# Kernel tuning notes

Hardware: AMD Instinct MI355X
Metric: run time of the kernel (lower is better)

The kernel has to match this reference:

```python
import jax, jax.numpy as jnp
import numpy as np

B, S, M, E, H, F, V, L = 2, 2048, 1024, 512, 8, 2048, 8192, 6


def setup_inputs() -> dict:
    key = jax.random.key(0)
    ks = iter(jax.random.split(key, 32))
    n = lambda shape, s=0.02: jax.random.normal(next(ks), shape, jnp.float32) * s
    return {
        "encoded": jax.random.normal(next(ks), (B, M, E), jnp.float32),
        "seq": jax.random.randint(next(ks), (B, S), 0, V, jnp.int32),
        "input_embed": n((V, E)),           # shared input/output embedding
        "pos_embed": n((S, E)),
        "output_bias": jnp.zeros((V,), jnp.float32),
        "self_in_w": n((L, 3 * E, E)), "self_in_b": jnp.zeros((L, 3 * E), jnp.float32),
        "self_out_w": n((L, E, E)), "self_out_b": jnp.zeros((L, E), jnp.float32),
        "cross_in_w": n((L, 3 * E, E)), "cross_in_b": jnp.zeros((L, 3 * E), jnp.float32),
        "cross_out_w": n((L, E, E)), "cross_out_b": jnp.zeros((L, E), jnp.float32),
        "self_norm_g": jnp.ones((L, E), jnp.float32), "self_norm_b": jnp.zeros((L, E), jnp.float32),
        "cross_norm_g": jnp.ones((L, E), jnp.float32), "cross_norm_b": jnp.zeros((L, E), jnp.float32),
        "mlp_norm_g": jnp.ones((L, E), jnp.float32), "mlp_norm_b": jnp.zeros((L, E), jnp.float32),
        "lin1_w": n((L, F, E)), "lin1_b": jnp.zeros((L, F), jnp.float32),
        "lin2_w": n((L, E, F)), "lin2_b": jnp.zeros((L, E), jnp.float32),
        "final_norm_g": jnp.ones((E,), jnp.float32), "final_norm_b": jnp.zeros((E,), jnp.float32),
    }


def _ln(x, g, b, eps=1e-5):
    m = jnp.mean(x, axis=-1, keepdims=True)
    v = jnp.mean((x - m) ** 2, axis=-1, keepdims=True)
    return (x - m) * jax.lax.rsqrt(v + eps) * g + b


def _mha(q, k, v, in_w, in_b, out_w, out_b, mask):
    # torch nn.MultiheadAttention (batch_first) with packed in_proj [3E, E]
    Ed = q.shape[-1]
    dh = Ed // H
    qp = q @ in_w[:Ed].T + in_b[:Ed]
    kp = k @ in_w[Ed:2 * Ed].T + in_b[Ed:2 * Ed]
    vp = v @ in_w[2 * Ed:].T + in_b[2 * Ed:]
    split = lambda t: t.reshape(t.shape[0], t.shape[1], H, dh).transpose(0, 2, 1, 3)
    qh, kh, vh = split(qp), split(kp), split(vp)  # [B, H, S, dh]
    scores = jnp.einsum('bhqd,bhkd->bhqk', qh, kh) / jnp.sqrt(jnp.float32(dh))
    if mask is not None:
        scores = jnp.where(mask, scores, jnp.float32(-1e9))
    attn = jax.nn.softmax(scores, axis=-1)
    o = jnp.einsum('bhqk,bhkd->bhqd', attn, vh)
    o = o.transpose(0, 2, 1, 3).reshape(q.shape[0], q.shape[1], Ed)
    return o @ out_w.T + out_b


def reference(encoded, seq, input_embed, pos_embed, output_bias,
              self_in_w, self_in_b, self_out_w, self_out_b,
              cross_in_w, cross_in_b, cross_out_w, cross_out_b,
              self_norm_g, self_norm_b, cross_norm_g, cross_norm_b,
              mlp_norm_g, mlp_norm_b, lin1_w, lin1_b, lin2_w, lin2_b,
              final_norm_g, final_norm_b):
    # TransformerDecoder.fit: teacher-forced forward (eval-mode dropout = identity)
    seq_len = seq.shape[1]
    x = input_embed[seq] + pos_embed[:seq_len]          # [B, S, E]
    causal = jnp.tril(jnp.ones((seq_len, seq_len), bool))
    for i in range(L):
        # post-norm decoder layer (norm_first=False)
        attn = _mha(x, x, x, self_in_w[i], self_in_b[i], self_out_w[i], self_out_b[i], causal)
        y = _ln(x + attn, self_norm_g[i], self_norm_b[i])
        cattn = _mha(y, encoded, encoded, cross_in_w[i], cross_in_b[i], cross_out_w[i], cross_out_b[i], None)
        y = _ln(y + cattn, cross_norm_g[i], cross_norm_b[i])
        h = jax.nn.gelu(y @ lin1_w[i].T + lin1_b[i], approximate=False)
        x = _ln(y + h @ lin2_w[i].T + lin2_b[i], mlp_norm_g[i], mlp_norm_b[i])
    x = _ln(x, final_norm_g, final_norm_b)               # decoder-final norm
    return x @ input_embed.T + output_bias               # shared output embedding
```

## Files before the change

kernel.cpp:

```cpp
#include <hip/hip_runtime.h>
#include <math.h>

typedef unsigned short u16;
typedef __attribute__((ext_vector_type(8))) unsigned short u16x8;
typedef __attribute__((ext_vector_type(8))) __bf16 bf16x8;
typedef __attribute__((ext_vector_type(4))) float f32x4;

constexpr int Bc = 2, Sc = 2048, Mc = 1024, Ec = 512, Hc = 8, DH = 64, Fc = 2048, Vc = 8192, Lc = 6;
constexpr int Nc = Bc * Sc;
constexpr int NMc = Bc * Mc;

__device__ __forceinline__ u16 f2b(float f) {
  __bf16 h = (__bf16)f;
  return __builtin_bit_cast(u16, h);
}

__device__ __forceinline__ f32x4 mfma16(bf16x8 a, bf16x8 b, f32x4 c) {
  return __builtin_amdgcn_mfma_f32_16x16x32_bf16(a, b, c, 0, 0, 0);
}

constexpr int C0 = 1179648;
constexpr int C1 = C0 + 393216;
constexpr int C2 = C1 + 1179648;
constexpr int C3 = C2 + 393216;
constexpr int C4 = C3 + 1572864;
constexpr int C5 = C4 + 1572864;
constexpr int C6 = C5 + 1048576;
constexpr int C7 = C6 + 262144;

__global__ __launch_bounds__(256) void k_cvt_all(
    const float* __restrict__ s0, const float* __restrict__ s1,
    const float* __restrict__ s2, const float* __restrict__ s3,
    const float* __restrict__ s4, const float* __restrict__ s5,
    const float* __restrict__ s6, const float* __restrict__ s7,
    u16* __restrict__ d0, u16* __restrict__ d1, u16* __restrict__ d2,
    u16* __restrict__ d3, u16* __restrict__ d4, u16* __restrict__ d5,
    u16* __restrict__ d6, u16* __restrict__ d7) {
  int i = blockIdx.x * 256 + threadIdx.x;
  const float* s; u16* d; int off;
  if (i < C3) {
    if (i < C1) { if (i < C0) { s = s0; d = d0; off = i; }
                  else        { s = s1; d = d1; off = i - C0; } }
    else        { if (i < C2) { s = s2; d = d2; off = i - C1; }
                  else        { s = s3; d = d3; off = i - C2; } }
  } else {
    if (i < C5) { if (i < C4) { s = s4; d = d4; off = i - C3; }
                  else        { s = s5; d = d5; off = i - C4; } }
    else        { if (i < C6) { s = s6; d = d6; off = i - C5; }
                  else        { s = s7; d = d7; off = i - C6; } }
  }
  float4 v = ((const float4*)s)[off];
  unsigned lo = (unsigned)f2b(v.x) | ((unsigned)f2b(v.y) << 16);
  unsigned hi = (unsigned)f2b(v.z) | ((unsigned)f2b(v.w) << 16);
  ((uint2*)d)[off] = make_uint2(lo, hi);
}

__global__ __launch_bounds__(256) void k_embed(const int* __restrict__ seq,
                                               const float* __restrict__ emb,
                                               const float* __restrict__ pos,
                                               float* __restrict__ x,
                                               u16* __restrict__ xb) {
  int idx = blockIdx.x * 256 + threadIdx.x;
  int row = idx >> 9, e = idx & 511;
  int s = row & (Sc - 1);
  float v = emb[(size_t)seq[row] * Ec + e] + pos[(size_t)s * Ec + e];
  x[idx] = v;
  xb[idx] = f2b(v);
}

template <int BM, int BN, int ACT>
__global__ __launch_bounds__(256) void k_gemm_bf(const u16* __restrict__ A,
                                                 const u16* __restrict__ W,
                                                 const float* __restrict__ bias,
                                                 float* __restrict__ C32,
                                                 u16* __restrict__ Cb,
                                                 int K, int Mo) {
  constexpr int WM = BM / 2, WN = BN / 2, FM = WM / 16, FN = WN / 16;
  __shared__ __attribute__((aligned(16))) u16 As[2][BM * 64];
  __shared__ __attribute__((aligned(16))) u16 Bs[2][BN * 64];
  const int tid = threadIdx.x;
  const int w = tid >> 6, l = tid & 63, l15 = l & 15, l4 = l >> 4;
  const int lr = l >> 3, lc = l & 7;
  const int wr = (w >> 1) * WM, wc = (w & 1) * WN;
  const size_t row0 = (size_t)blockIdx.y * BM, col0 = (size_t)blockIdx.x * BN;
  const u16* Ab = A + row0 * K;
  const u16* Wb = W + col0 * K;
  f32x4 acc[FM][FN] = {};

  auto stage = [&](int buf, int k0) {
#pragma unroll
    for (int i = 0; i < BM / 32; ++i) {
      int sw = lr ^ ((i * 4 + w) & 7);
      int row = i * 32 + w * 8 + lr;
      const u16* ga = Ab + (size_t)row * K + k0 + ((lc ^ sw) & 7) * 8;
      __builtin_amdgcn_global_load_lds((const __attribute__((address_space(1))) void*)ga,
          (__attribute__((address_space(3))) void*)((char*)As[buf] + (i * 32 + w * 8) * 128), 16, 0, 0);
    }
#pragma unroll
    for (int i = 0; i < BN / 32; ++i) {
      int sw = lr ^ ((i * 4 + w) & 7);
      int row = i * 32 + w * 8 + lr;
      const u16* gw = Wb + (size_t)row * K + k0 + ((lc ^ sw) & 7) * 8;
      __builtin_amdgcn_global_load_lds((const __attribute__((address_space(1))) void*)gw,
          (__attribute__((address_space(3))) void*)((char*)Bs[buf] + (i * 32 + w * 8) * 128), 16, 0, 0);
    }
  };

  const int nk = K / 64;
  stage(0, 0);
  int cur = 0;
  for (int kt = 0; kt < nk; ++kt) {
    __syncthreads();
    if (kt + 1 < nk) stage(cur ^ 1, (kt + 1) * 64);
    const u16* AsC = As[cur];
    const u16* BsC = Bs[cur];
#pragma unroll
    for (int ks = 0; ks < 2; ++ks) {
      bf16x8 af[FM], bfr[FN];
#pragma unroll
      for (int m = 0; m < FM; ++m) {
        int ra = wr + m * 16 + l15;
        int sw = (l15 & 7) ^ ((wr / 8 + 2 * m + (l15 >> 3)) & 7);
        af[m] = *(const bf16x8*)&AsC[ra * 64 + ((ks * 32 + l4 * 8) ^ (sw * 8))];
      }
#pragma unroll
      for (int n = 0; n < FN; ++n) {
        int rb = wc + n * 16 + l15;
        int sw = (l15 & 7) ^ ((wc / 8 + 2 * n + (l15 >> 3)) & 7);
        bfr[n] = *(const bf16x8*)&BsC[rb * 64 + ((ks * 32 + l4 * 8) ^ (sw * 8))];
      }
#pragma unroll
      for (int m = 0; m < FM; ++m)
#pragma unroll
        for (int n = 0; n < FN; ++n)
          acc[m][n] = mfma16(af[m], bfr[n], acc[m][n]);
    }
    cur ^= 1;
  }
#pragma unroll
  for (int n = 0; n < FN; ++n) {
    size_t col = col0 + wc + n * 16 + l15;
    float bv = bias[col];
#pragma unroll
    for (int m = 0; m < FM; ++m)
#pragma unroll
      for (int r = 0; r < 4; ++r) {
        size_t row = row0 + wr + m * 16 + l4 * 4 + r;
        float v = acc[m][n][r] + bv;
        if (ACT) v = 0.5f * v * (1.f + erff(v * 0.70710678118654752f));
        if (C32) C32[row * Mo + col] = v;
        if (Cb) Cb[row * Mo + col] = f2b(v);
      }
  }
}

__global__ __launch_bounds__(512, 4) void k_flash(const u16* __restrict__ Qp, int sq,
                                                  const u16* __restrict__ Kp,
                                                  const u16* __restrict__ Vp, int skv,
                                                  u16* __restrict__ Op, int so,
                                                  int Sq, int Sk, int causal) {
  __shared__ __attribute__((aligned(16))) u16 Kst[4][64 * 64];
  __shared__ __attribute__((aligned(16))) u16 Vt[4][64 * 64];
  __shared__ __attribute__((aligned(16))) u16 Pl[8][16 * 64];
  const int tid = threadIdx.x;
  const int w = tid >> 6, l = tid & 63, l15 = l & 15, l4 = l >> 4;
  const int wq = w & 3, ws = w >> 2;
  const int lr = l >> 3, lc = l & 7;
  const int t256 = tid & 255;
  const int kk2 = t256 >> 3, dblk = tid & 7;
  const int nqt = Sq / 64, nkt = Sk / 64;
  const int h = blockIdx.y, b = blockIdx.z;
  const int bx = blockIdx.x;
  const int qi = causal ? ((b & 1) ? bx : (nqt - 1 - bx)) : bx;
  const int qt0 = qi * 64;
  const int nt = causal ? (qi + 1) : nkt;
  const int NI = (nt + 1) >> 1;
  const u16* Qb = Qp + (size_t)b * Sq * sq + h * DH;
  const u16* Kb = Kp + (size_t)b * Sk * skv + h * DH;
  const u16* Vb = Vp + (size_t)b * Sk * skv + h * DH;
  const int qg = qt0 + wq * 16 + l15;

  bf16x8 qf[2];
  {
    const u16* qp0 = Qb + (size_t)qg * sq + l4 * 8;
    qf[0] = *(const bf16x8*)(qp0);
    qf[1] = *(const bf16x8*)(qp0 + 32);
  }

  f32x4 oacc[4] = {};
  float ls = 0.f, Mx = -3e38f;
  const float CSC = 0.18033688011112042f;
  const int swp = (l15 & 7) ^ (l15 >> 3);

  u16x8 va, vbv;
  auto stageK = [&](int slot, int kt) {
#pragma unroll
    for (int i = 0; i < 2; ++i) {
      int sw = lr ^ ((i * 4 + wq) & 7);
      int row = i * 32 + wq * 8 + lr;
      const u16* src = Kb + (size_t)(kt + row) * skv + ((lc ^ sw) & 7) * 8;
      __builtin_amdgcn_global_load_lds((const __attribute__((address_space(1))) void*)src,
          (__attribute__((address_space(3))) void*)((char*)Kst[slot] + (i * 32 + wq * 8) * 128), 16, 0, 0);
    }
  };
  auto loadV = [&](int kt) {
    const u16* vp0 = Vb + (size_t)(kt + 2 * kk2) * skv + dblk * 8;
    va = *(const u16x8*)vp0;
    vbv = *(const u16x8*)(vp0 + skv);
  };
  auto writeV = [&](int slot) {
    char* Vb_ = (char*)Vt[slot];
#pragma unroll
    for (int j = 0; j < 8; ++j) {
      int d = dblk * 8 + j;
      int sw = (j ^ dblk) & 7;
      unsigned pk = (unsigned)va[j] | ((unsigned)vbv[j] << 16);
      *(unsigned*)(Vb_ + d * 128 + ((4 * kk2) ^ (sw << 4))) = pk;
    }
  };

  stageK(ws * 2, ws * 64);
  loadV(ws * 64);
  writeV(ws * 2);
  asm volatile("s_waitcnt lgkmcnt(0)" ::: "memory");
  __builtin_amdgcn_sched_barrier(0);
  __builtin_amdgcn_s_barrier();

  u16* Pw = Pl[w];
  for (int i = 0; i < NI; ++i) {
    const int t = 2 * i + ws;
    const int tn = t + 2;
    const int cur = ws * 2 + (i & 1);
    const int nxt = ws * 2 + ((i + 1) & 1);
    const bool haveNext = tn < nt;
    if (haveNext) {
      stageK(nxt, tn * 64);
      loadV(tn * 64);
    }
    if (t < nt) {
      const u16* KstC = Kst[cur];
      const u16* VtC = Vt[cur];

      f32x4 sf[4] = {};
      __builtin_amdgcn_s_setprio(1);
#pragma unroll
      for (int n = 0; n < 4; ++n) {
        int rk = n * 16 + l15;
        int sw = (l15 & 7) ^ ((2 * n + (l15 >> 3)) & 7);
#pragma unroll
        for (int ks = 0; ks < 2; ++ks) {
          bf16x8 kf = *(const bf16x8*)&KstC[rk * 64 + ((ks * 32 + l4 * 8) ^ (sw * 8))];
          sf[n] = mfma16(kf, qf[ks], sf[n]);
        }
      }
      __builtin_amdgcn_s_setprio(0);

      if (causal && t == nt - 1) {
#pragma unroll
        for (int n = 0; n < 4; ++n)
#pragma unroll
          for (int r = 0; r < 4; ++r) {
            int kcol = t * 64 + n * 16 + l4 * 4 + r;
            if (kcol > qg) sf[n][r] = -3e38f;
          }
      }

      float tm = fmaxf(fmaxf(fmaxf(sf[0][0], sf[0][1]), fmaxf(sf[0][2], sf[0][3])),
                       fmaxf(fmaxf(sf[1][0], sf[1][1]), fmaxf(sf[1][2], sf[1][3])));
      tm = fmaxf(tm, fmaxf(fmaxf(fmaxf(sf[2][0], sf[2][1]), fmaxf(sf[2][2], sf[2][3])),
                           fmaxf(fmaxf(sf[3][0], sf[3][1]), fmaxf(sf[3][2], sf[3][3]))));
      tm = fmaxf(tm, __shfl_xor(tm, 16, 64));
      tm = fmaxf(tm, __shfl_xor(tm, 32, 64));
      float Mn = fmaxf(Mx, tm);
      float al = exp2f((Mx - Mn) * CSC);
      Mx = Mn;
      float mxc = Mx * CSC;

      float rs = 0.f;
#pragma unroll
      for (int n = 0; n < 4; ++n) {
        float p0 = exp2f(sf[n][0] * CSC - mxc);
        float p1 = exp2f(sf[n][1] * CSC - mxc);
        float p2 = exp2f(sf[n][2] * CSC - mxc);
        float p3 = exp2f(sf[n][3] * CSC - mxc);
        rs += (p0 + p1) + (p2 + p3);
        unsigned w0 = (unsigned)f2b(p0) | ((unsigned)f2b(p1) << 16);
        unsigned w1 = (unsigned)f2b(p2) | ((unsigned)f2b(p3) << 16);
        int bb = (n * 32 + l4 * 8) ^ (swp << 4);
        *(unsigned*)((char*)Pw + l15 * 128 + bb) = w0;
        *(unsigned*)((char*)Pw + l15 * 128 + bb + 4) = w1;
      }
      rs += __shfl_xor(rs, 16, 64);
      rs += __shfl_xor(rs, 32, 64);
      ls = ls * al + rs;

      if (__any(al < 1.f)) {
        float a0 = __shfl(al, l4 * 4 + 0, 64);
        float a1 = __shfl(al, l4 * 4 + 1, 64);
        float a2 = __shfl(al, l4 * 4 + 2, 64);
        float a3 = __shfl(al, l4 * 4 + 3, 64);
#pragma unroll
        for (int n2 = 0; n2 < 4; ++n2) {
          oacc[n2][0] *= a0; oacc[n2][1] *= a1;
          oacc[n2][2] *= a2; oacc[n2][3] *= a3;
        }
      }

      asm volatile("s_waitcnt lgkmcnt(0)" ::: "memory");
      __builtin_amdgcn_sched_barrier(0);

      __builtin_amdgcn_s_setprio(1);
#pragma unroll
      for (int ks = 0; ks < 2; ++ks) {
        bf16x8 pf = *(const bf16x8*)((char*)Pw + l15 * 128 + ((ks * 64 + l4 * 16) ^ (swp << 4)));
#pragma unroll
        for (int n2 = 0; n2 < 4; ++n2) {
          int rd = n2 * 16 + l15;
          int sw = (l15 & 7) ^ ((2 * n2 + (l15 >> 3)) & 7);
          bf16x8 vf = *(const bf16x8*)((char*)VtC + rd * 128 + ((ks * 64 + l4 * 16) ^ (sw << 4)));
          oacc[n2] = mfma16(pf, vf, oacc[n2]);
        }
      }
      __builtin_amdgcn_s_setprio(0);
    }

    if (haveNext) writeV(nxt);
    asm volatile("s_waitcnt lgkmcnt(0)" ::: "memory");
    __builtin_amdgcn_sched_barrier(0);
    __builtin_amdgcn_s_barrier();
  }

  __syncthreads();
  float* OB = (float*)&Kst[0][0];
  float* ML = (float*)&Vt[0][0];
  if (l4 == 0) {
    ML[ws * 64 + wq * 16 + l15] = Mx;
    ML[128 + ws * 64 + wq * 16 + l15] = ls;
  }
  if (ws == 1) {
#pragma unroll
    for (int n2 = 0; n2 < 4; ++n2)
#pragma unroll
      for (int r = 0; r < 4; ++r)
        OB[(wq * 16 + l4 * 4 + r) * 64 + n2 * 16 + l15] = oacc[n2][r];
  }
  __syncthreads();
  if (ws == 0) {
    u16* Ob = Op + (size_t)b * Sq * so + h * DH;
#pragma unroll
    for (int r = 0; r < 4; ++r) {
      int qs = wq * 16 + l4 * 4 + r;
      float mA = ML[qs], mB = ML[64 + qs];
      float lA = ML[128 + qs], lB = ML[192 + qs];
      float M = fmaxf(mA, mB);
      float aA = exp2f((mA - M) * CSC);
      float aB = exp2f((mB - M) * CSC);
      float inv = 1.f / (lA * aA + lB * aB);
      int qrow = qt0 + qs;
#pragma unroll
      for (int n2 = 0; n2 < 4; ++n2) {
        float o = (oacc[n2][r] * aA + OB[qs * 64 + n2 * 16 + l15] * aB) * inv;
        Ob[(size_t)qrow * so + n2 * 16 + l15] = f2b(o);
      }
    }
  }
}

__global__ __launch_bounds__(256) void k_res_ln(const float* __restrict__ xin,
                                                const float* __restrict__ rres,
                                                const float* __restrict__ g,
                                                const float* __restrict__ bet,
                                                float* __restrict__ outf,
                                                u16* __restrict__ outb,
                                                int has_res) {
  __shared__ float red[4];
  const int row = blockIdx.x, tid = threadIdx.x;
  const float2* xr = (const float2*)(xin + (size_t)row * Ec);
  float2 v = xr[tid];
  if (has_res) {
    float2 rv = ((const float2*)(rres + (size_t)row * Ec))[tid];
    v.x += rv.x; v.y += rv.y;
  }
  float s = v.x + v.y;
#pragma unroll
  for (int o = 32; o; o >>= 1) s += __shfl_down(s, o, 64);
  if ((tid & 63) == 0) red[tid >> 6] = s;
  __syncthreads();
  const float mean = (red[0] + red[1] + red[2] + red[3]) * (1.f / Ec);
  float d0 = v.x - mean, d1 = v.y - mean;
  float vs = d0 * d0 + d1 * d1;
#pragma unroll
  for (int o = 32; o; o >>= 1) vs += __shfl_down(vs, o, 64);
  __syncthreads();
  if ((tid & 63) == 0) red[tid >> 6] = vs;
  __syncthreads();
  const float var = (red[0] + red[1] + red[2] + red[3]) * (1.f / Ec);
  const float inv = rsqrtf(var + 1e-5f);
  float2 gv = ((const float2*)g)[tid];
  float2 bv = ((const float2*)bet)[tid];
  float o0 = d0 * inv * gv.x + bv.x;
  float o1 = d1 * inv * gv.y + bv.y;
  ((float2*)(outf + (size_t)row * Ec))[tid] = make_float2(o0, o1);
  if (outb) {
    unsigned pk = (unsigned)f2b(o0) | ((unsigned)f2b(o1) << 16);
    ((unsigned*)(outb + (size_t)row * Ec))[tid] = pk;
  }
}

extern "C" void kernel_launch(void* const* d_in, const int* in_sizes, int n_in,
                              void* d_out, int out_size, void* d_ws, size_t ws_size,
                              hipStream_t stream) {
  const float* encoded      = (const float*)d_in[0];
  const int*   seq          = (const int*)d_in[1];
  const float* input_embed  = (const float*)d_in[2];
  const float* pos_embed    = (const float*)d_in[3];
  const float* output_bias  = (const float*)d_in[4];
  const float* self_in_w    = (const float*)d_in[5];
  const float* self_in_b    = (const float*)d_in[6];
  const float* self_out_w   = (const float*)d_in[7];
  const float* self_out_b   = (const float*)d_in[8];
  const float* cross_in_w   = (const float*)d_in[9];
  const float* cross_in_b   = (const float*)d_in[10];
  const float* cross_out_w  = (const float*)d_in[11];
  const float* cross_out_b  = (const float*)d_in[12];
  const float* self_norm_g  = (const float*)d_in[13];
  const float* self_norm_b  = (const float*)d_in[14];
  const float* cross_norm_g = (const float*)d_in[15];
  const float* cross_norm_b = (const float*)d_in[16];
  const float* mlp_norm_g   = (const float*)d_in[17];
  const float* mlp_norm_b   = (const float*)d_in[18];
  const float* lin1_w       = (const float*)d_in[19];
  const float* lin1_b       = (const float*)d_in[20];
  const float* lin2_w       = (const float*)d_in[21];
  const float* lin2_b       = (const float*)d_in[22];
  const float* final_norm_g = (const float*)d_in[23];
  const float* final_norm_b = (const float*)d_in[24];

  char* oc = (char*)d_out;
  auto take = [&](size_t bytes) { char* p = oc; oc += bytes; return p; };
  u16* wsi  = (u16*)take((size_t)Lc * 3 * Ec * Ec * 2);
  u16* wso  = (u16*)take((size_t)Lc * Ec * Ec * 2);
  u16* wci  = (u16*)take((size_t)Lc * 3 * Ec * Ec * 2);
  u16* wco  = (u16*)take((size_t)Lc * Ec * Ec * 2);
  u16* wl1  = (u16*)take((size_t)Lc * Fc * Ec * 2);
  u16* wl2  = (u16*)take((size_t)Lc * Ec * Fc * 2);
  u16* encb = (u16*)take((size_t)NMc * Ec * 2);
  float* xs  = (float*)take((size_t)Nc * Ec * 4);
  float* ys  = (float*)take((size_t)Nc * Ec * 4);
  float* tmp = (float*)take((size_t)Nc * Ec * 4);
  u16* xbf  = (u16*)take((size_t)Nc * Ec * 2);
  u16* qkvb = (u16*)take((size_t)Nc * 3 * Ec * 2);
  u16* ctxb = (u16*)take((size_t)Nc * Ec * 2);
  u16* qxb  = (u16*)take((size_t)Nc * Ec * 2);
  u16* kvb  = (u16*)take((size_t)NMc * 2 * Ec * 2);
  u16* hbf  = (u16*)take((size_t)Nc * Fc * 2);
  u16* xfb  = (u16*)d_ws;
  u16* embb = (u16*)((char*)d_ws + (size_t)Nc * Ec * 2);

  const dim3 blk(256);
  k_cvt_all<<<dim3(29696), blk, 0, stream>>>(
      self_in_w, self_out_w, cross_in_w, cross_out_w, lin1_w, lin2_w,
      input_embed, encoded, wsi, wso, wci, wco, wl1, wl2, embb, encb);

  k_embed<<<dim3(Nc * Ec / 256), blk, 0, stream>>>(seq, input_embed, pos_embed, xs, xbf);

  const dim3 gAttn(Sc / 64, Hc, Bc);
  const dim3 blkA(512);
  for (int l = 0; l < Lc; ++l) {
    const u16* wsi_l = wsi + (size_t)l * 3 * Ec * Ec;
    const u16* wci_l = wci + (size_t)l * 3 * Ec * Ec;
    k_gemm_bf<128, 64, 0><<<dim3(3 * Ec / 64, Nc / 128), blk, 0, stream>>>(
        xbf, wsi_l, self_in_b + (size_t)l * 3 * Ec, nullptr, qkvb, Ec, 3 * Ec);
    k_flash<<<gAttn, blkA, 0, stream>>>(qkvb, 3 * Ec, qkvb + Ec, qkvb + 2 * Ec, 3 * Ec,
                                        ctxb, Ec, Sc, Sc, 1);
    k_gemm_bf<64, 64, 0><<<dim3(Ec / 64, Nc / 64), blk, 0, stream>>>(
        ctxb, wso + (size_t)l * Ec * Ec, self_out_b + (size_t)l * Ec, tmp, nullptr, Ec, Ec);
    k_res_ln<<<dim3(Nc), blk, 0, stream>>>(xs, tmp, self_norm_g + (size_t)l * Ec,
                                           self_norm_b + (size_t)l * Ec, ys, xbf, 1);
    k_gemm_bf<64, 64, 0><<<dim3(Ec / 64, Nc / 64), blk, 0, stream>>>(
        xbf, wci_l, cross_in_b + (size_t)l * 3 * Ec, nullptr, qxb, Ec, Ec);
    k_gemm_bf<64, 64, 0><<<dim3(2 * Ec / 64, NMc / 64), blk, 0, stream>>>(
        encb, wci_l + (size_t)Ec * Ec, cross_in_b + (size_t)l * 3 * Ec + Ec,
        nullptr, kvb, Ec, 2 * Ec);
    k_flash<<<gAttn, blkA, 0, stream>>>(qxb, Ec, kvb, kvb + Ec, 2 * Ec,
                                        ctxb, Ec, Sc, Mc, 0);
    k_gemm_bf<64, 64, 0><<<dim3(Ec / 64, Nc / 64), blk, 0, stream>>>(
        ctxb, wco + (size_t)l * Ec * Ec, cross_out_b + (size_t)l * Ec, tmp, nullptr, Ec, Ec);
    k_res_ln<<<dim3(Nc), blk, 0, stream>>>(ys, tmp, cross_norm_g + (size_t)l * Ec,
                                           cross_norm_b + (size_t)l * Ec, xs, xbf, 1);
    k_gemm_bf<128, 128, 1><<<dim3(Fc / 128, Nc / 128), blk, 0, stream>>>(
        xbf, wl1 + (size_t)l * Fc * Ec, lin1_b + (size_t)l * Fc, nullptr, hbf, Ec, Fc);
    k_gemm_bf<64, 64, 0><<<dim3(Ec / 64, Nc / 64), blk, 0, stream>>>(
        hbf, wl2 + (size_t)l * Ec * Fc, lin2_b + (size_t)l * Ec, tmp, nullptr, Fc, Ec);
    k_res_ln<<<dim3(Nc), blk, 0, stream>>>(xs, tmp, mlp_norm_g + (size_t)l * Ec,
                                           mlp_norm_b + (size_t)l * Ec, xs, xbf, 1);
  }

  k_res_ln<<<dim3(Nc), blk, 0, stream>>>(xs, nullptr, final_norm_g, final_norm_b, xs, xfb, 0);
  k_gemm_bf<128, 128, 0><<<dim3(Vc / 128, Nc / 128), blk, 0, stream>>>(
      xfb, embb, output_bias, (float*)d_out, nullptr, Ec, Vc);
}
```

Baseline: 1.177 ms.

## Add XCD-aware tile swizzle, merge cross-attn projections, warp-per-row layernorm

```diff
diff --git a/kernel.cpp b/kernel.cpp
--- a/kernel.cpp
+++ b/kernel.cpp
@@ -69,12 +69,13 @@
 }
 
 template <int BM, int BN, int ACT>
-__global__ __launch_bounds__(256) void k_gemm_bf(const u16* __restrict__ A,
-                                                 const u16* __restrict__ W,
-                                                 const float* __restrict__ bias,
-                                                 float* __restrict__ C32,
-                                                 u16* __restrict__ Cb,
-                                                 int K, int Mo) {
+__device__ __forceinline__ void gemm_body(const u16* __restrict__ A,
+                                          const u16* __restrict__ W,
+                                          const float* __restrict__ bias,
+                                          float* __restrict__ C32,
+                                          u16* __restrict__ Cb,
+                                          int K, int Mo,
+                                          size_t row0, size_t col0) {
   constexpr int WM = BM / 2, WN = BN / 2, FM = WM / 16, FN = WN / 16;
   __shared__ __attribute__((aligned(16))) u16 As[2][BM * 64];
   __shared__ __attribute__((aligned(16))) u16 Bs[2][BN * 64];
@@ -82,7 +83,6 @@
   const int w = tid >> 6, l = tid & 63, l15 = l & 15, l4 = l >> 4;
   const int lr = l >> 3, lc = l & 7;
   const int wr = (w >> 1) * WM, wc = (w & 1) * WN;
-  const size_t row0 = (size_t)blockIdx.y * BM, col0 = (size_t)blockIdx.x * BN;
   const u16* Ab = A + row0 * K;
   const u16* Wb = W + col0 * K;
   f32x4 acc[FM][FN] = {};
@@ -105,6 +105,31 @@
           (__attribute__((address_space(3))) void*)((char*)Bs[buf] + (i * 32 + w * 8) * 128), 16, 0, 0);
     }
   };
+  auto compute = [&](int buf) {
+    const u16* AsC = As[buf];
+    const u16* BsC = Bs[buf];
+#pragma unroll
+    for (int ks = 0; ks < 2; ++ks) {
+      bf16x8 af[FM], bfr[FN];
+#pragma unroll
+      for (int m = 0; m < FM; ++m) {
+        int ra = wr + m * 16 + l15;
+        int sw = (l15 & 7) ^ ((wr / 8 + 2 * m + (l15 >> 3)) & 7);
+        af[m] = *(const bf16x8*)&AsC[ra * 64 + ((ks * 32 + l4 * 8) ^ (sw * 8))];
+      }
+#pragma unroll
+      for (int n = 0; n < FN; ++n) {
+        int rb = wc + n * 16 + l15;
+        int sw = (l15 & 7) ^ ((wc / 8 + 2 * n + (l15 >> 3)) & 7);
+        bfr[n] = *(const bf16x8*)&BsC[rb * 64 + ((ks * 32 + l4 * 8) ^ (sw * 8))];
+      }
+#pragma unroll
+      for (int m = 0; m < FM; ++m)
+#pragma unroll
+        for (int n = 0; n < FN; ++n)
+          acc[m][n] = mfma16(af[m], bfr[n], acc[m][n]);
+    }
+  };
 
   const int nk = K / 64;
   stage(0, 0);
@@ -112,31 +137,10 @@
   for (int kt = 0; kt < nk; ++kt) {
     __syncthreads();
     if (kt + 1 < nk) stage(cur ^ 1, (kt + 1) * 64);
-    const u16* AsC = As[cur];
-    const u16* BsC = Bs[cur];
-#pragma unroll
-    for (int ks = 0; ks < 2; ++ks) {
-      bf16x8 af[FM], bfr[FN];
-#pragma unroll
-      for (int m = 0; m < FM; ++m) {
-        int ra = wr + m * 16 + l15;
-        int sw = (l15 & 7) ^ ((wr / 8 + 2 * m + (l15 >> 3)) & 7);
-        af[m] = *(const bf16x8*)&AsC[ra * 64 + ((ks * 32 + l4 * 8) ^ (sw * 8))];
-      }
-#pragma unroll
-      for (int n = 0; n < FN; ++n) {
-        int rb = wc + n * 16 + l15;
-        int sw = (l15 & 7) ^ ((wc / 8 + 2 * n + (l15 >> 3)) & 7);
-        bfr[n] = *(const bf16x8*)&BsC[rb * 64 + ((ks * 32 + l4 * 8) ^ (sw * 8))];
-      }
-#pragma unroll
-      for (int m = 0; m < FM; ++m)
-#pragma unroll
-        for (int n = 0; n < FN; ++n)
-          acc[m][n] = mfma16(af[m], bfr[n], acc[m][n]);
-    }
+    compute(cur);
     cur ^= 1;
   }
+
 #pragma unroll
   for (int n = 0; n < FN; ++n) {
     size_t col = col0 + wc + n * 16 + l15;
@@ -151,6 +155,44 @@
         if (C32) C32[row * Mo + col] = v;
         if (Cb) Cb[row * Mo + col] = f2b(v);
       }
+  }
+}
+
+template <int BM, int BN, int ACT, int XS>
+__global__ __launch_bounds__(256) void k_gemm_bf(const u16* __restrict__ A,
+                                                 const u16* __restrict__ W,
+                                                 const float* __restrict__ bias,
+                                                 float* __restrict__ C32,
+                                                 u16* __restrict__ Cb,
+                                                 int K, int Mo) {
+  int bx, by;
+  if constexpr (XS) {
+    int gx = gridDim.x;
+    int bid = blockIdx.x + gx * blockIdx.y;
+    int cw = gx >> 3;
+    int xcd = bid & 7, j = bid >> 3;
+    bx = xcd * cw + (j % cw);
+    by = j / cw;
+  } else {
+    bx = blockIdx.x; by = blockIdx.y;
+  }
+  gemm_body<BM, BN, ACT>(A, W, bias, C32, Cb, K, Mo, (size_t)by * BM, (size_t)bx * BN);
+}
+
+__global__ __launch_bounds__(256) void k_gemm_cross(
+    const u16* __restrict__ A0, const u16* __restrict__ W0, const float* __restrict__ b0,
+    u16* __restrict__ Co0,
+    const u16* __restrict__ A1, const u16* __restrict__ W1, const float* __restrict__ b1,
+    u16* __restrict__ Co1) {
+  int bid = blockIdx.x;
+  if (bid < 512) {
+    int xcd = bid & 7, j = bid >> 3;
+    gemm_body<64, 64, 0>(A0, W0, b0, nullptr, Co0, Ec, Ec, (size_t)j * 64, (size_t)xcd * 64);
+  } else {
+    int r = bid - 512;
+    int xcd = r & 7, j = r >> 3;
+    int bx = xcd * 2 + (j & 1), by = j >> 1;
+    gemm_body<64, 64, 0>(A1, W1, b1, nullptr, Co1, Ec, 2 * Ec, (size_t)by * 64, (size_t)bx * 64);
   }
 }
 
@@ -373,37 +415,43 @@
                                                 float* __restrict__ outf,
                                                 u16* __restrict__ outb,
                                                 int has_res) {
-  __shared__ float red[4];
-  const int row = blockIdx.x, tid = threadIdx.x;
-  const float2* xr = (const float2*)(xin + (size_t)row * Ec);
-  float2 v = xr[tid];
+  const int tid = threadIdx.x, w = tid >> 6, l = tid & 63;
+  const int row = blockIdx.x * 4 + w;
+  const float4* xr = (const float4*)(xin + (size_t)row * Ec);
+  float4 a = xr[2 * l], c = xr[2 * l + 1];
   if (has_res) {
-    float2 rv = ((const float2*)(rres + (size_t)row * Ec))[tid];
-    v.x += rv.x; v.y += rv.y;
-  }
-  float s = v.x + v.y;
-#pragma unroll
-  for (int o = 32; o; o >>= 1) s += __shfl_down(s, o, 64);
-  if ((tid & 63) == 0) red[tid >> 6] = s;
-  __syncthreads();
-  const float mean = (red[0] + red[1] + red[2] + red[3]) * (1.f / Ec);
-  float d0 = v.x - mean, d1 = v.y - mean;
-  float vs = d0 * d0 + d1 * d1;
-#pragma unroll
-  for (int o = 32; o; o >>= 1) vs += __shfl_down(vs, o, 64);
-  __syncthreads();
-  if ((tid & 63) == 0) red[tid >> 6] = vs;
-  __syncthreads();
-  const float var = (red[0] + red[1] + red[2] + red[3]) * (1.f / Ec);
-  const float inv = rsqrtf(var + 1e-5f);
-  float2 gv = ((const float2*)g)[tid];
-  float2 bv = ((const float2*)bet)[tid];
-  float o0 = d0 * inv * gv.x + bv.x;
-  float o1 = d1 * inv * gv.y + bv.y;
-  ((float2*)(outf + (size_t)row * Ec))[tid] = make_float2(o0, o1);
+    const float4* rr = (const float4*)(rres + (size_t)row * Ec);
+    float4 r0 = rr[2 * l], r1 = rr[2 * l + 1];
+    a.x += r0.x; a.y += r0.y; a.z += r0.z; a.w += r0.w;
+    c.x += r1.x; c.y += r1.y; c.z += r1.z; c.w += r1.w;
+  }
+  float s = (a.x + a.y) + (a.z + a.w) + (c.x + c.y) + (c.z + c.w);
+#pragma unroll
+  for (int o = 32; o; o >>= 1) s += __shfl_xor(s, o, 64);
+  const float mean = s * (1.f / Ec);
+  float d0 = a.x - mean, d1 = a.y - mean, d2 = a.z - mean, d3 = a.w - mean;
+  float e0 = c.x - mean, e1 = c.y - mean, e2 = c.z - mean, e3 = c.w - mean;
+  float vs = d0 * d0 + d1 * d1 + d2 * d2 + d3 * d3 +
+             e0 * e0 + e1 * e1 + e2 * e2 + e3 * e3;
+#pragma unroll
+  for (int o = 32; o; o >>= 1) vs += __shfl_xor(vs, o, 64);
+  const float inv = rsqrtf(vs * (1.f / Ec) + 1e-5f);
+  float4 g0 = ((const float4*)g)[2 * l], g1 = ((const float4*)g)[2 * l + 1];
+  float4 b0 = ((const float4*)bet)[2 * l], b1 = ((const float4*)bet)[2 * l + 1];
+  float o0 = d0 * inv * g0.x + b0.x, o1 = d1 * inv * g0.y + b0.y;
+  float o2 = d2 * inv * g0.z + b0.z, o3 = d3 * inv * g0.w + b0.w;
+  float o4 = e0 * inv * g1.x + b1.x, o5 = e1 * inv * g1.y + b1.y;
+  float o6 = e2 * inv * g1.z + b1.z, o7 = e3 * inv * g1.w + b1.w;
+  float4* orow = (float4*)(outf + (size_t)row * Ec);
+  orow[2 * l] = make_float4(o0, o1, o2, o3);
+  orow[2 * l + 1] = make_float4(o4, o5, o6, o7);
   if (outb) {
-    unsigned pk = (unsigned)f2b(o0) | ((unsigned)f2b(o1) << 16);
-    ((unsigned*)(outb + (size_t)row * Ec))[tid] = pk;
+    uint4 pk;
+    pk.x = (unsigned)f2b(o0) | ((unsigned)f2b(o1) << 16);
+    pk.y = (unsigned)f2b(o2) | ((unsigned)f2b(o3) << 16);
+    pk.z = (unsigned)f2b(o4) | ((unsigned)f2b(o5) << 16);
+    pk.w = (unsigned)f2b(o6) | ((unsigned)f2b(o7) << 16);
+    ((uint4*)(outb + (size_t)row * Ec))[l] = pk;
   }
 }
 
@@ -466,37 +514,36 @@
 
   const dim3 gAttn(Sc / 64, Hc, Bc);
   const dim3 blkA(512);
+  const dim3 gLN(Nc / 4);
   for (int l = 0; l < Lc; ++l) {
     const u16* wsi_l = wsi + (size_t)l * 3 * Ec * Ec;
     const u16* wci_l = wci + (size_t)l * 3 * Ec * Ec;
-    k_gemm_bf<128, 64, 0><<<dim3(3 * Ec / 64, Nc / 128), blk, 0, stream>>>(
+    k_gemm_bf<128, 64, 0, 1><<<dim3(3 * Ec / 64, Nc / 128), blk, 0, stream>>>(
         xbf, wsi_l, self_in_b + (size_t)l * 3 * Ec, nullptr, qkvb, Ec, 3 * Ec);
     k_flash<<<gAttn, blkA, 0, stream>>>(qkvb, 3 * Ec, qkvb + Ec, qkvb + 2 * Ec, 3 * Ec,
                                         ctxb, Ec, Sc, Sc, 1);
-    k_gemm_bf<64, 64, 0><<<dim3(Ec / 64, Nc / 64), blk, 0, stream>>>(
+    k_gemm_bf<64, 64, 0, 1><<<dim3(Ec / 64, Nc / 64), blk, 0, stream>>>(
         ctxb, wso + (size_t)l * Ec * Ec, self_out_b + (size_t)l * Ec, tmp, nullptr, Ec, Ec);
-    k_res_ln<<<dim3(Nc), blk, 0, stream>>>(xs, tmp, self_norm_g + (size_t)l * Ec,
-                                           self_norm_b + (size_t)l * Ec, ys, xbf, 1);
-    k_gemm_bf<64, 64, 0><<<dim3(Ec / 64, Nc / 64), blk, 0, stream>>>(
-        xbf, wci_l, cross_in_b + (size_t)l * 3 * Ec, nullptr, qxb, Ec, Ec);
-    k_gemm_bf<64, 64, 0><<<dim3(2 * Ec / 64, NMc / 64), blk, 0, stream>>>(
-        encb, wci_l + (size_t)Ec * Ec, cross_in_b + (size_t)l * 3 * Ec + Ec,
-        nullptr, kvb, Ec, 2 * Ec);
+    k_res_ln<<<gLN, blk, 0, stream>>>(xs, tmp, self_norm_g + (size_t)l * Ec,
+                                      self_norm_b + (size_t)l * Ec, ys, xbf, 1);
+    k_gemm_cross<<<dim3(1024), blk, 0, stream>>>(
+        xbf, wci_l, cross_in_b + (size_t)l * 3 * Ec, qxb,
+        encb, wci_l + (size_t)Ec * Ec, cross_in_b + (size_t)l * 3 * Ec + Ec, kvb);
     k_flash<<<gAttn, blkA, 0, stream>>>(qxb, Ec, kvb, kvb + Ec, 2 * Ec,
                                         ctxb, Ec, Sc, Mc, 0);
-    k_gemm_bf<64, 64, 0><<<dim3(Ec / 64, Nc / 64), blk, 0, stream>>>(
+    k_gemm_bf<64, 64, 0, 1><<<dim3(Ec / 64, Nc / 64), blk, 0, stream>>>(
         ctxb, wco + (size_t)l * Ec * Ec, cross_out_b + (size_t)l * Ec, tmp, nullptr, Ec, Ec);
-    k_res_ln<<<dim3(Nc), blk, 0, stream>>>(ys, tmp, cross_norm_g + (size_t)l * Ec,
-                                           cross_norm_b + (size_t)l * Ec, xs, xbf, 1);
-    k_gemm_bf<128, 128, 1><<<dim3(Fc / 128, Nc / 128), blk, 0, stream>>>(
+    k_res_ln<<<gLN, blk, 0, stream>>>(ys, tmp, cross_norm_g + (size_t)l * Ec,
+                                      cross_norm_b + (size_t)l * Ec, xs, xbf, 1);
+    k_gemm_bf<128, 128, 1, 1><<<dim3(Fc / 128, Nc / 128), blk, 0, stream>>>(
         xbf, wl1 + (size_t)l * Fc * Ec, lin1_b + (size_t)l * Fc, nullptr, hbf, Ec, Fc);
-    k_gemm_bf<64, 64, 0><<<dim3(Ec / 64, Nc / 64), blk, 0, stream>>>(
+    k_gemm_bf<64, 64, 0, 1><<<dim3(Ec / 64, Nc / 64), blk, 0, stream>>>(
         hbf, wl2 + (size_t)l * Ec * Fc, lin2_b + (size_t)l * Ec, tmp, nullptr, Fc, Ec);
-    k_res_ln<<<dim3(Nc), blk, 0, stream>>>(xs, tmp, mlp_norm_g + (size_t)l * Ec,
-                                           mlp_norm_b + (size_t)l * Ec, xs, xbf, 1);
-  }
-
-  k_res_ln<<<dim3(Nc), blk, 0, stream>>>(xs, nullptr, final_norm_g, final_norm_b, xs, xfb, 0);
-  k_gemm_bf<128, 128, 0><<<dim3(Vc / 128, Nc / 128), blk, 0, stream>>>(
+    k_res_ln<<<gLN, blk, 0, stream>>>(xs, tmp, mlp_norm_g + (size_t)l * Ec,
+                                      mlp_norm_b + (size_t)l * Ec, xs, xbf, 1);
+  }
+
+  k_res_ln<<<gLN, blk, 0, stream>>>(xs, nullptr, final_norm_g, final_norm_b, xs, xfb, 0);
+  k_gemm_bf<128, 128, 0, 1><<<dim3(Vc / 128, Nc / 128), blk, 0, stream>>>(
       xfb, embb, output_bias, (float*)d_out, nullptr, Ec, Vc);
 }
```

After: 1.141 ms. 3.1% less time.
